# Kernel optimization log

Measured on AMD Instinct MI355X. Metric: run time of the kernel, lower is better.

The kernel has to match this reference:

```python
import jax, jax.numpy as jnp
import numpy as np

N_NODES = 50000
N_EDGES = 400000
N_GRAPHS = 128
IN_DIM = 768
HID = 128
N_CLASSES = 11
BN_EPS = 1e-5


def _sage_conv(x, src, dst, Wl, bl, Wr):
    # PyG SAGEConv (aggr='mean'): out = lin_l(mean_{j->i} x_j) + lin_r(x_i)
    # messages flow src -> dst; nodes with no in-edges get a zero aggregate.
    n = x.shape[0]
    deg = jax.ops.segment_sum(jnp.ones_like(dst, x.dtype), dst, num_segments=n)
    agg = jax.ops.segment_sum(x[src], dst, num_segments=n)  # [N, d] gather+scatter
    agg = agg / jnp.maximum(deg, 1.0)[:, None]
    return agg @ Wl.T + bl + x @ Wr.T


def _batch_norm(x, gamma, beta):
    # training-mode BatchNorm1d: biased batch statistics over the node axis
    m = jnp.mean(x, axis=0)
    v = jnp.var(x, axis=0)
    return (x - m) * jax.lax.rsqrt(v + BN_EPS) * gamma + beta


def setup_inputs() -> dict:
    key = jax.random.key(0)
    ks = jax.random.split(key, 16)
    x = jax.random.normal(ks[0], (N_NODES, IN_DIM), dtype=jnp.float32)
    edge_index = jax.random.randint(ks[1], (2, N_EDGES), 0, N_NODES, dtype=jnp.int32)
    batch = jnp.sort(jax.random.randint(ks[2], (N_NODES,), 0, N_GRAPHS, dtype=jnp.int32))

    def lin_w(k, out_d, in_d):
        return jax.random.normal(k, (out_d, in_d), dtype=jnp.float32) * (1.0 / np.sqrt(in_d))

    params = {
        'W1l': lin_w(ks[3], HID, IN_DIM), 'b1': jnp.zeros((HID,), jnp.float32),
        'W1r': lin_w(ks[4], HID, IN_DIM),
        'g1': jnp.ones((HID,), jnp.float32), 'be1': jnp.zeros((HID,), jnp.float32),
        'W2l': lin_w(ks[5], HID, HID), 'b2': jnp.zeros((HID,), jnp.float32),
        'W2r': lin_w(ks[6], HID, HID),
        'g2': jnp.ones((HID,), jnp.float32), 'be2': jnp.zeros((HID,), jnp.float32),
        'W3l': lin_w(ks[7], HID, HID), 'b3': jnp.zeros((HID,), jnp.float32),
        'W3r': lin_w(ks[8], HID, HID),
        'g3': jnp.ones((HID,), jnp.float32), 'be3': jnp.zeros((HID,), jnp.float32),
        'Wlin': lin_w(ks[9], N_CLASSES, HID), 'blin': jnp.zeros((N_CLASSES,), jnp.float32),
    }
    return {'x': x, 'edge_index': edge_index, 'batch': batch, **params}


def reference(x, edge_index, batch,
              W1l, b1, W1r, g1, be1,
              W2l, b2, W2r, g2, be2,
              W3l, b3, W3r, g3, be3,
              Wlin, blin):
    src, dst = edge_index[0], edge_index[1]
    h = jax.nn.relu(_batch_norm(_sage_conv(x, src, dst, W1l, b1, W1r), g1, be1))
    h = jax.nn.relu(_batch_norm(_sage_conv(h, src, dst, W2l, b2, W2r), g2, be2))
    h = _batch_norm(_sage_conv(h, src, dst, W3l, b3, W3r), g3, be3)
    # global_max_pool over graph ids
    pooled = jax.ops.segment_max(h, batch, num_segments=N_GRAPHS)  # [G, HID]
    # dropout is identity at inference
    return pooled @ Wlin.T + blin  # [G, 11]
```

## Files before the change

kernel.cpp:

```cpp
#include <hip/hip_runtime.h>

#define N_NODESC 50000
#define N_EDGESC 400000
#define N_GRAPHSC 128
#define IN_DIMC 768
#define HIDC 128
#define NCLSC 11
#define BN_EPSC 1e-5f
#define NB_AGG 8
#define NREP 64
#define SCAN_NB ((N_NODESC + 255) / 256)

typedef __bf16 bf16_t;
typedef __bf16 bf16x8 __attribute__((ext_vector_type(8)));
typedef float f32x4 __attribute__((ext_vector_type(4)));

__device__ inline f32x4 mfma_16x16x32_bf16(bf16x8 a, bf16x8 b, f32x4 c) {
    return __builtin_amdgcn_mfma_f32_16x16x32_bf16(a, b, c, 0, 0, 0);
}

template<bool APPLY_BN>
__global__ __launch_bounds__(256) void gemm_kernel(const float* __restrict__ A,
                                                   const float* __restrict__ Bl,
                                                   const float* __restrict__ Br,
                                                   const float* __restrict__ sc,
                                                   bf16_t* __restrict__ Cl,
                                                   float* __restrict__ Cr, int M, int K)
{
    __shared__ bf16_t As[128][40];
    __shared__ bf16_t Bs[128][40];

    const int t  = threadIdx.x;
    const int m0 = blockIdx.x * 128;
    const float* Bsel = (blockIdx.y == 0) ? Bl : Br;

    const int r  = t >> 3;
    const int c4 = (t & 7) * 4;

    const int wid  = t >> 6;
    const int lane = t & 63;
    const int wm   = (wid >> 1) * 64;
    const int wn   = (wid & 1) * 64;
    const int l16  = lane & 15;
    const int quad = lane >> 4;

    f32x4 acc[4][4] = {};

    for (int k0 = 0; k0 < K; k0 += 32) {
#pragma unroll
        for (int p = 0; p < 4; p++) {
            int row = r + p * 32;
            int am  = m0 + row; if (am > M - 1) am = M - 1;
            float4 v = *(const float4*)&A[(size_t)am * K + k0 + c4];
            if (APPLY_BN) {
                float4 s4 = *(const float4*)&sc[k0 + c4];
                float4 h4 = *(const float4*)&sc[HIDC + k0 + c4];
                v.x = fmaxf(fmaf(v.x, s4.x, h4.x), 0.0f);
                v.y = fmaxf(fmaf(v.y, s4.y, h4.y), 0.0f);
                v.z = fmaxf(fmaf(v.z, s4.z, h4.z), 0.0f);
                v.w = fmaxf(fmaf(v.w, s4.w, h4.w), 0.0f);
            }
            As[row][c4 + 0] = (bf16_t)v.x; As[row][c4 + 1] = (bf16_t)v.y;
            As[row][c4 + 2] = (bf16_t)v.z; As[row][c4 + 3] = (bf16_t)v.w;
            float4 w = *(const float4*)&Bsel[(size_t)row * K + k0 + c4];
            Bs[row][c4 + 0] = (bf16_t)w.x; Bs[row][c4 + 1] = (bf16_t)w.y;
            Bs[row][c4 + 2] = (bf16_t)w.z; Bs[row][c4 + 3] = (bf16_t)w.w;
        }
        __syncthreads();

        bf16x8 af[4], bfr[4];
#pragma unroll
        for (int i = 0; i < 4; i++)
            af[i] = *(const bf16x8*)&As[wm + i * 16 + l16][quad * 8];
#pragma unroll
        for (int j = 0; j < 4; j++)
            bfr[j] = *(const bf16x8*)&Bs[wn + j * 16 + l16][quad * 8];
#pragma unroll
        for (int i = 0; i < 4; i++)
#pragma unroll
            for (int j = 0; j < 4; j++)
                acc[i][j] = mfma_16x16x32_bf16(af[i], bfr[j], acc[i][j]);
        __syncthreads();
    }

#pragma unroll
    for (int i = 0; i < 4; i++) {
        int rowb = m0 + wm + i * 16 + quad * 4;
#pragma unroll
        for (int j = 0; j < 4; j++) {
            int colh = wn + j * 16 + l16;
#pragma unroll
            for (int rr = 0; rr < 4; rr++) {
                int row = rowb + rr;
                if (row < M) {
                    if (blockIdx.y == 0) Cl[(size_t)row * HIDC + colh] = (bf16_t)acc[i][j][rr];
                    else                 Cr[(size_t)row * HIDC + colh] = acc[i][j][rr];
                }
            }
        }
    }
}

__global__ void degi_kernel(const int* __restrict__ ei, int* __restrict__ degi) {
    int e = blockIdx.x * blockDim.x + threadIdx.x;
    if (e < N_EDGESC) atomicAdd(&degi[ei[N_EDGESC + e]], 1);
}

__global__ __launch_bounds__(256) void scan1_kernel(const int* __restrict__ degi,
                                                    int* __restrict__ local,
                                                    int* __restrict__ partials)
{
    __shared__ int tmp[256];
    const int t = threadIdx.x;
    const int i = blockIdx.x * 256 + t;
    int v = (i < N_NODESC) ? degi[i] : 0;
    tmp[t] = v;
    __syncthreads();
    for (int off = 1; off < 256; off <<= 1) {
        int u = (t >= off) ? tmp[t - off] : 0;
        __syncthreads();
        tmp[t] += u;
        __syncthreads();
    }
    if (i < N_NODESC) local[i] = tmp[t] - v;
    if (t == 255) partials[blockIdx.x] = tmp[255];
}

__global__ __launch_bounds__(256) void scan2_kernel(int* __restrict__ partials)
{
    __shared__ int tmp[256];
    const int t = threadIdx.x;
    int v = (t < SCAN_NB) ? partials[t] : 0;
    tmp[t] = v;
    __syncthreads();
    for (int off = 1; off < 256; off <<= 1) {
        int u = (t >= off) ? tmp[t - off] : 0;
        __syncthreads();
        tmp[t] += u;
        __syncthreads();
    }
    if (t < SCAN_NB) partials[t] = tmp[t] - v;
}

__global__ __launch_bounds__(256) void scan3_kernel(const int* __restrict__ local,
                                                    const int* __restrict__ partials,
                                                    int* __restrict__ rowptr,
                                                    int* __restrict__ cursor)
{
    const int i = blockIdx.x * 256 + threadIdx.x;
    if (i < N_NODESC) {
        int r = local[i] + partials[blockIdx.x];
        rowptr[i] = r;
        cursor[i] = r;
    }
    if (i == 0) rowptr[N_NODESC] = N_EDGESC;
}

__global__ void fill_kernel(const int* __restrict__ ei, int* __restrict__ cursor,
                            int* __restrict__ col) {
    int e = blockIdx.x * blockDim.x + threadIdx.x;
    if (e >= N_EDGESC) return;
    int d = ei[N_EDGESC + e];
    int pos = atomicAdd(&cursor[d], 1);
    col[pos] = ei[e];
}

__global__ __launch_bounds__(128) void agg_combine_kernel(const int* __restrict__ rowptr,
                                                          const int* __restrict__ col,
                                                          const bf16_t* __restrict__ Plb,
                                                          const float* __restrict__ Pr,
                                                          const float* __restrict__ bias,
                                                          float* __restrict__ Hpre,
                                                          float* __restrict__ stats, int M)
{
    const int c = threadIdx.x;
    const float b = bias[c];
    float s = 0.f, s2 = 0.f;
    const int n0 = blockIdx.x * NB_AGG;
    for (int rr = 0; rr < NB_AGG; rr++) {
        int n = n0 + rr;
        if (n >= M) break;
        int lo = rowptr[n], hi = rowptr[n + 1];
        float a = 0.f;
        for (int e = lo; e < hi; e += 8) {
            int rem = hi - e;
            int idx[8];
#pragma unroll
            for (int j = 0; j < 8; j++) {
                int ee = e + j; if (ee > hi - 1) ee = hi - 1;
                idx[j] = col[ee];
            }
            float v[8];
#pragma unroll
            for (int j = 0; j < 8; j++)
                v[j] = (float)Plb[(size_t)idx[j] * HIDC + c];
#pragma unroll
            for (int j = 0; j < 8; j++)
                if (j < rem) a += v[j];
        }
        int d = hi - lo;
        float inv = 1.0f / (float)(d > 0 ? d : 1);
        float pre = fmaf(a, inv, b) + Pr[(size_t)n * HIDC + c];
        Hpre[(size_t)n * HIDC + c] = pre;
        s += pre; s2 += pre * pre;
    }
    const int rep = blockIdx.x & (NREP - 1);
    atomicAdd(&stats[rep * 256 + c], s);
    atomicAdd(&stats[rep * 256 + HIDC + c], s2);
}

__global__ __launch_bounds__(128) void finalize_kernel(const float* __restrict__ stats,
                                                       const float* __restrict__ g,
                                                       const float* __restrict__ be,
                                                       float* __restrict__ sc, int M)
{
    int c = threadIdx.x;
    float sum = 0.f, sumsq = 0.f;
    for (int r = 0; r < NREP; r++) {
        sum   += stats[r * 256 + c];
        sumsq += stats[r * 256 + HIDC + c];
    }
    float invM = 1.0f / (float)M;
    float mean = sum * invM;
    float var  = sumsq * invM - mean * mean;
    float s = rsqrtf(var + BN_EPSC) * g[c];
    sc[c] = s;
    sc[HIDC + c] = be[c] - mean * s;
}

__global__ __launch_bounds__(128) void pool_kernel(const float* __restrict__ Hpre,
                                                   const float* __restrict__ sc,
                                                   const int* __restrict__ batch,
                                                   float* __restrict__ pooled, int M)
{
    int gph = blockIdx.x;
    int c   = threadIdx.x;
    float s = sc[c], h = sc[HIDC + c];
    int lo = 0, hi = M;
    while (lo < hi) { int m = (lo + hi) >> 1; if (batch[m] < gph) lo = m + 1; else hi = m; }
    int lo2 = lo, hi2 = M;
    while (lo2 < hi2) { int m = (lo2 + hi2) >> 1; if (batch[m] < gph + 1) lo2 = m + 1; else hi2 = m; }
    float mx = -INFINITY;
    for (int rr = lo; rr < lo2; rr++)
        mx = fmaxf(mx, fmaf(Hpre[(size_t)rr * HIDC + c], s, h));
    pooled[gph * HIDC + c] = mx;
}

__global__ __launch_bounds__(128) void final_kernel(const float* __restrict__ pooled,
                                                    const float* __restrict__ W,
                                                    const float* __restrict__ bl,
                                                    float* __restrict__ out)
{
    __shared__ float sp[HIDC];
    int gph = blockIdx.x;
    int t   = threadIdx.x;
    sp[t] = pooled[gph * HIDC + t];
    __syncthreads();
    if (t < NCLSC) {
        float acc = bl[t];
        for (int c = 0; c < HIDC; c++) acc += sp[c] * W[t * HIDC + c];
        out[gph * NCLSC + t] = acc;
    }
}

extern "C" void kernel_launch(void* const* d_in, const int* in_sizes, int n_in,
                              void* d_out, int out_size, void* d_ws, size_t ws_size,
                              hipStream_t stream)
{
    const float* x     = (const float*)d_in[0];
    const int*   ei    = (const int*)d_in[1];
    const int*   batch = (const int*)d_in[2];
    const float* W1l = (const float*)d_in[3];
    const float* b1  = (const float*)d_in[4];
    const float* W1r = (const float*)d_in[5];
    const float* g1  = (const float*)d_in[6];
    const float* be1 = (const float*)d_in[7];
    const float* W2l = (const float*)d_in[8];
    const float* b2  = (const float*)d_in[9];
    const float* W2r = (const float*)d_in[10];
    const float* g2  = (const float*)d_in[11];
    const float* be2 = (const float*)d_in[12];
    const float* W3l = (const float*)d_in[13];
    const float* b3  = (const float*)d_in[14];
    const float* W3r = (const float*)d_in[15];
    const float* g3  = (const float*)d_in[16];
    const float* be3 = (const float*)d_in[17];
    const float* Wlin = (const float*)d_in[18];
    const float* blin = (const float*)d_in[19];

    const int M = N_NODESC;

    char* w = (char*)d_ws;
    bf16_t* Plb  = (bf16_t*)w;  w += (size_t)M * HIDC * 2;
    float* Pr    = (float*)w;   w += (size_t)M * HIDC * 4;
    float* Hpre  = (float*)w;   w += (size_t)M * HIDC * 4;
    int*   rowptr= (int*)w;     w += (size_t)(M + 16) * 4;
    int*   col   = (int*)w;     w += (size_t)N_EDGESC * 4;
    int*   cursor= (int*)w;     w += (size_t)M * 4;
    int*   degi  = (int*)w;     w += (size_t)M * 4;
    int*   slocal= (int*)w;     w += (size_t)M * 4;
    int*   spart = (int*)w;     w += 256 * 4;
    float* stats = (float*)w;   w += (size_t)NREP * 256 * 4;
    float* sc    = (float*)w;   w += 256 * 4;
    float* pooled= (float*)w;   w += (size_t)N_GRAPHSC * HIDC * 4;

    const dim3 gemm_grid((M + 127) / 128, 2);
    const int agg_blocks = (M + NB_AGG - 1) / NB_AGG;
    const size_t stats_bytes = (size_t)NREP * 256 * 4;

    hipMemsetAsync(degi, 0, (size_t)M * 4, stream);
    degi_kernel<<<(N_EDGESC + 255) / 256, 256, 0, stream>>>(ei, degi);
    scan1_kernel<<<SCAN_NB, 256, 0, stream>>>(degi, slocal, spart);
    scan2_kernel<<<1, 256, 0, stream>>>(spart);
    scan3_kernel<<<SCAN_NB, 256, 0, stream>>>(slocal, spart, rowptr, cursor);
    fill_kernel<<<(N_EDGESC + 255) / 256, 256, 0, stream>>>(ei, cursor, col);

    gemm_kernel<false><<<gemm_grid, 256, 0, stream>>>(x, W1l, W1r, nullptr, Plb, Pr, M, IN_DIMC);
    hipMemsetAsync(stats, 0, stats_bytes, stream);
    agg_combine_kernel<<<agg_blocks, 128, 0, stream>>>(rowptr, col, Plb, Pr, b1, Hpre, stats, M);
    finalize_kernel<<<1, 128, 0, stream>>>(stats, g1, be1, sc, M);

    gemm_kernel<true><<<gemm_grid, 256, 0, stream>>>(Hpre, W2l, W2r, sc, Plb, Pr, M, HIDC);
    hipMemsetAsync(stats, 0, stats_bytes, stream);
    agg_combine_kernel<<<agg_blocks, 128, 0, stream>>>(rowptr, col, Plb, Pr, b2, Hpre, stats, M);
    finalize_kernel<<<1, 128, 0, stream>>>(stats, g2, be2, sc, M);

    gemm_kernel<true><<<gemm_grid, 256, 0, stream>>>(Hpre, W3l, W3r, sc, Plb, Pr, M, HIDC);
    hipMemsetAsync(stats, 0, stats_bytes, stream);
    agg_combine_kernel<<<agg_blocks, 128, 0, stream>>>(rowptr, col, Plb, Pr, b3, Hpre, stats, M);
    finalize_kernel<<<1, 128, 0, stream>>>(stats, g3, be3, sc, M);

    pool_kernel<<<N_GRAPHSC, 128, 0, stream>>>(Hpre, sc, batch, pooled, M);
    final_kernel<<<N_GRAPHSC, 128, 0, stream>>>(pooled, Wlin, blin, (float*)d_out);
}
```

Baseline: 595.2 us.

## Load GEMM tiles via global_load_lds with swizzle, store intermediates in bf16

The GEMM now copies A and B tiles straight into swizzled LDS using the global_load_lds builtin. Conversion to bf16 and the BN+ReLU step happen after the LDS read instead of during staging through registers. Weights are converted to bf16 once per call by a small kernel. The right-branch projection and the pre-BN activations are now stored in bf16 instead of fp32, halving the traffic in the aggregation and pooling kernels at some cost in precision.

```diff
diff --git a/kernel.cpp b/kernel.cpp
--- a/kernel.cpp
+++ b/kernel.cpp
@@ -15,28 +15,35 @@
 typedef __bf16 bf16x8 __attribute__((ext_vector_type(8)));
 typedef float f32x4 __attribute__((ext_vector_type(4)));
 
-__device__ inline f32x4 mfma_16x16x32_bf16(bf16x8 a, bf16x8 b, f32x4 c) {
+typedef __attribute__((address_space(1))) void glb_void;
+typedef __attribute__((address_space(3))) void lds_void;
+
+__device__ __forceinline__ void cp16(const void* g, void* l) {
+    __builtin_amdgcn_global_load_lds((glb_void*)g, (lds_void*)l, 16, 0, 0);
+}
+
+__device__ __forceinline__ f32x4 mfma_16x16x32_bf16(bf16x8 a, bf16x8 b, f32x4 c) {
     return __builtin_amdgcn_mfma_f32_16x16x32_bf16(a, b, c, 0, 0, 0);
 }
 
-template<bool APPLY_BN>
-__global__ __launch_bounds__(256) void gemm_kernel(const float* __restrict__ A,
-                                                   const float* __restrict__ Bl,
-                                                   const float* __restrict__ Br,
+template<int MODE>
+__global__ __launch_bounds__(256) void gemm_kernel(const void* __restrict__ Av,
+                                                   const bf16_t* __restrict__ Wb,
                                                    const float* __restrict__ sc,
                                                    bf16_t* __restrict__ Cl,
-                                                   float* __restrict__ Cr, int M, int K)
-{
-    __shared__ bf16_t As[128][40];
-    __shared__ bf16_t Bs[128][40];
-
-    const int t  = threadIdx.x;
-    const int m0 = blockIdx.x * 128;
-    const float* Bsel = (blockIdx.y == 0) ? Bl : Br;
-
-    const int r  = t >> 3;
-    const int c4 = (t & 7) * 4;
-
+                                                   bf16_t* __restrict__ Cr,
+                                                   int M, int K)
+{
+    constexpr int ABYTES = (MODE == 0) ? 128 * 32 * 4 : 128 * 32 * 2;
+    constexpr int AISS   = (MODE == 0) ? 4 : 2;
+    constexpr int AESZ   = (MODE == 0) ? 4 : 2;
+    __shared__ __align__(16) unsigned char smem[ABYTES + 128 * 32 * 2];
+    unsigned char* Asm = smem;
+    unsigned char* Bsm = smem + ABYTES;
+
+    const int t    = threadIdx.x;
+    const int m0   = blockIdx.x * 128;
+    const int half = blockIdx.y;
     const int wid  = t >> 6;
     const int lane = t & 63;
     const int wm   = (wid >> 1) * 64;
@@ -44,37 +51,83 @@
     const int l16  = lane & 15;
     const int quad = lane >> 4;
 
+    const char* aSrc[AISS]; int aDst[AISS];
+#pragma unroll
+    for (int s = 0; s < AISS; s++) {
+        int L = (s * 4 + wid) * 64 + lane;
+        int r, c;
+        if (MODE == 0) { r = L >> 3; c = (L & 7) ^ (r & 7); }
+        else           { r = L >> 2; c = (L & 3) ^ ((r >> 1) & 3); }
+        int row = m0 + r; if (row > M - 1) row = M - 1;
+        aSrc[s] = (const char*)Av + ((size_t)row * K + (size_t)c * (16 / AESZ)) * AESZ;
+        aDst[s] = (s * 4 + wid) * 1024;
+    }
+    const char* bSrc[2]; int bDst[2];
+#pragma unroll
+    for (int s = 0; s < 2; s++) {
+        int L = (s * 4 + wid) * 64 + lane;
+        int r = L >> 2;
+        int c = (L & 3) ^ ((r >> 1) & 3);
+        bSrc[s] = (const char*)(Wb + (size_t)(half * 128 + r) * K + c * 8);
+        bDst[s] = (s * 4 + wid) * 1024;
+    }
+
+    int aOff[4][2], bOff[4];
+#pragma unroll
+    for (int i = 0; i < 4; i++) {
+        int ra = wm + i * 16 + l16;
+        if (MODE == 0) {
+            aOff[i][0] = ra * 128 + (((2 * quad)     ^ (ra & 7)) * 16);
+            aOff[i][1] = ra * 128 + (((2 * quad + 1) ^ (ra & 7)) * 16);
+        } else {
+            aOff[i][0] = ra * 64 + ((quad ^ ((ra >> 1) & 3)) * 16);
+            aOff[i][1] = 0;
+        }
+        int rb = wn + i * 16 + l16;
+        bOff[i] = rb * 64 + ((quad ^ ((rb >> 1) & 3)) * 16);
+    }
+
     f32x4 acc[4][4] = {};
 
     for (int k0 = 0; k0 < K; k0 += 32) {
 #pragma unroll
-        for (int p = 0; p < 4; p++) {
-            int row = r + p * 32;
-            int am  = m0 + row; if (am > M - 1) am = M - 1;
-            float4 v = *(const float4*)&A[(size_t)am * K + k0 + c4];
-            if (APPLY_BN) {
-                float4 s4 = *(const float4*)&sc[k0 + c4];
-                float4 h4 = *(const float4*)&sc[HIDC + k0 + c4];
-                v.x = fmaxf(fmaf(v.x, s4.x, h4.x), 0.0f);
-                v.y = fmaxf(fmaf(v.y, s4.y, h4.y), 0.0f);
-                v.z = fmaxf(fmaf(v.z, s4.z, h4.z), 0.0f);
-                v.w = fmaxf(fmaf(v.w, s4.w, h4.w), 0.0f);
+        for (int s = 0; s < AISS; s++)
+            cp16(aSrc[s] + (size_t)k0 * AESZ, Asm + aDst[s]);
+#pragma unroll
+        for (int s = 0; s < 2; s++)
+            cp16(bSrc[s] + (size_t)k0 * 2, Bsm + bDst[s]);
+        __syncthreads();
+
+        bf16x8 af[4], bfr[4];
+        if (MODE == 0) {
+#pragma unroll
+            for (int i = 0; i < 4; i++) {
+                float4 u0 = *(const float4*)(Asm + aOff[i][0]);
+                float4 u1 = *(const float4*)(Asm + aOff[i][1]);
+                af[i][0] = (bf16_t)u0.x; af[i][1] = (bf16_t)u0.y;
+                af[i][2] = (bf16_t)u0.z; af[i][3] = (bf16_t)u0.w;
+                af[i][4] = (bf16_t)u1.x; af[i][5] = (bf16_t)u1.y;
+                af[i][6] = (bf16_t)u1.z; af[i][7] = (bf16_t)u1.w;
             }
-            As[row][c4 + 0] = (bf16_t)v.x; As[row][c4 + 1] = (bf16_t)v.y;
-            As[row][c4 + 2] = (bf16_t)v.z; As[row][c4 + 3] = (bf16_t)v.w;
-            float4 w = *(const float4*)&Bsel[(size_t)row * K + k0 + c4];
-            Bs[row][c4 + 0] = (bf16_t)w.x; Bs[row][c4 + 1] = (bf16_t)w.y;
-            Bs[row][c4 + 2] = (bf16_t)w.z; Bs[row][c4 + 3] = (bf16_t)w.w;
+        } else {
+            const int ch0 = k0 + quad * 8;
+            float4 s0 = *(const float4*)&sc[ch0];
+            float4 s1 = *(const float4*)&sc[ch0 + 4];
+            float4 h0 = *(const float4*)&sc[HIDC + ch0];
+            float4 h1 = *(const float4*)&sc[HIDC + ch0 + 4];
+            float ss[8] = {s0.x, s0.y, s0.z, s0.w, s1.x, s1.y, s1.z, s1.w};
+            float hh[8] = {h0.x, h0.y, h0.z, h0.w, h1.x, h1.y, h1.z, h1.w};
+#pragma unroll
+            for (int i = 0; i < 4; i++) {
+                bf16x8 raw = *(const bf16x8*)(Asm + aOff[i][0]);
+#pragma unroll
+                for (int e = 0; e < 8; e++)
+                    af[i][e] = (bf16_t)fmaxf(fmaf((float)raw[e], ss[e], hh[e]), 0.0f);
+            }
         }
-        __syncthreads();
-
-        bf16x8 af[4], bfr[4];
-#pragma unroll
-        for (int i = 0; i < 4; i++)
-            af[i] = *(const bf16x8*)&As[wm + i * 16 + l16][quad * 8];
 #pragma unroll
         for (int j = 0; j < 4; j++)
-            bfr[j] = *(const bf16x8*)&Bs[wn + j * 16 + l16][quad * 8];
+            bfr[j] = *(const bf16x8*)(Bsm + bOff[j]);
 #pragma unroll
         for (int i = 0; i < 4; i++)
 #pragma unroll
@@ -83,6 +136,7 @@
         __syncthreads();
     }
 
+    bf16_t* C = half ? Cr : Cl;
 #pragma unroll
     for (int i = 0; i < 4; i++) {
         int rowb = m0 + wm + i * 16 + quad * 4;
@@ -92,13 +146,18 @@
 #pragma unroll
             for (int rr = 0; rr < 4; rr++) {
                 int row = rowb + rr;
-                if (row < M) {
-                    if (blockIdx.y == 0) Cl[(size_t)row * HIDC + colh] = (bf16_t)acc[i][j][rr];
-                    else                 Cr[(size_t)row * HIDC + colh] = acc[i][j][rr];
-                }
+                if (row < M) C[(size_t)row * HIDC + colh] = (bf16_t)acc[i][j][rr];
             }
         }
     }
+}
+
+__global__ void wconv_kernel(const float* __restrict__ Wl, const float* __restrict__ Wr,
+                             bf16_t* __restrict__ out, int KN)
+{
+    int i = blockIdx.x * blockDim.x + threadIdx.x;
+    if (i < KN)           out[i] = (bf16_t)Wl[i];
+    else if (i < 2 * KN)  out[i] = (bf16_t)Wr[i - KN];
 }
 
 __global__ void degi_kernel(const int* __restrict__ ei, int* __restrict__ degi) {
@@ -168,9 +227,9 @@
 __global__ __launch_bounds__(128) void agg_combine_kernel(const int* __restrict__ rowptr,
                                                           const int* __restrict__ col,
                                                           const bf16_t* __restrict__ Plb,
-                                                          const float* __restrict__ Pr,
+                                                          const bf16_t* __restrict__ Prb,
                                                           const float* __restrict__ bias,
-                                                          float* __restrict__ Hpre,
+                                                          bf16_t* __restrict__ Hb,
                                                           float* __restrict__ stats, int M)
 {
     const int c = threadIdx.x;
@@ -200,8 +259,8 @@
         }
         int d = hi - lo;
         float inv = 1.0f / (float)(d > 0 ? d : 1);
-        float pre = fmaf(a, inv, b) + Pr[(size_t)n * HIDC + c];
-        Hpre[(size_t)n * HIDC + c] = pre;
+        float pre = fmaf(a, inv, b) + (float)Prb[(size_t)n * HIDC + c];
+        Hb[(size_t)n * HIDC + c] = (bf16_t)pre;
         s += pre; s2 += pre * pre;
     }
     const int rep = blockIdx.x & (NREP - 1);
@@ -228,7 +287,7 @@
     sc[HIDC + c] = be[c] - mean * s;
 }
 
-__global__ __launch_bounds__(128) void pool_kernel(const float* __restrict__ Hpre,
+__global__ __launch_bounds__(128) void pool_kernel(const bf16_t* __restrict__ Hb,
                                                    const float* __restrict__ sc,
                                                    const int* __restrict__ batch,
                                                    float* __restrict__ pooled, int M)
@@ -242,7 +301,7 @@
     while (lo2 < hi2) { int m = (lo2 + hi2) >> 1; if (batch[m] < gph + 1) lo2 = m + 1; else hi2 = m; }
     float mx = -INFINITY;
     for (int rr = lo; rr < lo2; rr++)
-        mx = fmaxf(mx, fmaf(Hpre[(size_t)rr * HIDC + c], s, h));
+        mx = fmaxf(mx, fmaf((float)Hb[(size_t)rr * HIDC + c], s, h));
     pooled[gph * HIDC + c] = mx;
 }
 
@@ -292,8 +351,11 @@
 
     char* w = (char*)d_ws;
     bf16_t* Plb  = (bf16_t*)w;  w += (size_t)M * HIDC * 2;
-    float* Pr    = (float*)w;   w += (size_t)M * HIDC * 4;
-    float* Hpre  = (float*)w;   w += (size_t)M * HIDC * 4;
+    bf16_t* Prb  = (bf16_t*)w;  w += (size_t)M * HIDC * 2;
+    bf16_t* Hb   = (bf16_t*)w;  w += (size_t)M * HIDC * 2;
+    bf16_t* Wb1  = (bf16_t*)w;  w += (size_t)256 * IN_DIMC * 2;
+    bf16_t* Wb2  = (bf16_t*)w;  w += (size_t)256 * HIDC * 2;
+    bf16_t* Wb3  = (bf16_t*)w;  w += (size_t)256 * HIDC * 2;
     int*   rowptr= (int*)w;     w += (size_t)(M + 16) * 4;
     int*   col   = (int*)w;     w += (size_t)N_EDGESC * 4;
     int*   cursor= (int*)w;     w += (size_t)M * 4;
@@ -308,6 +370,10 @@
     const int agg_blocks = (M + NB_AGG - 1) / NB_AGG;
     const size_t stats_bytes = (size_t)NREP * 256 * 4;
 
+    wconv_kernel<<<(2 * 128 * IN_DIMC + 255) / 256, 256, 0, stream>>>(W1l, W1r, Wb1, 128 * IN_DIMC);
+    wconv_kernel<<<(2 * 128 * HIDC + 255) / 256, 256, 0, stream>>>(W2l, W2r, Wb2, 128 * HIDC);
+    wconv_kernel<<<(2 * 128 * HIDC + 255) / 256, 256, 0, stream>>>(W3l, W3r, Wb3, 128 * HIDC);
+
     hipMemsetAsync(degi, 0, (size_t)M * 4, stream);
     degi_kernel<<<(N_EDGESC + 255) / 256, 256, 0, stream>>>(ei, degi);
     scan1_kernel<<<SCAN_NB, 256, 0, stream>>>(degi, slocal, spart);
@@ -315,21 +381,21 @@
     scan3_kernel<<<SCAN_NB, 256, 0, stream>>>(slocal, spart, rowptr, cursor);
     fill_kernel<<<(N_EDGESC + 255) / 256, 256, 0, stream>>>(ei, cursor, col);
 
-    gemm_kernel<false><<<gemm_grid, 256, 0, stream>>>(x, W1l, W1r, nullptr, Plb, Pr, M, IN_DIMC);
+    gemm_kernel<0><<<gemm_grid, 256, 0, stream>>>(x, Wb1, nullptr, Plb, Prb, M, IN_DIMC);
     hipMemsetAsync(stats, 0, stats_bytes, stream);
-    agg_combine_kernel<<<agg_blocks, 128, 0, stream>>>(rowptr, col, Plb, Pr, b1, Hpre, stats, M);
+    agg_combine_kernel<<<agg_blocks, 128, 0, stream>>>(rowptr, col, Plb, Prb, b1, Hb, stats, M);
     finalize_kernel<<<1, 128, 0, stream>>>(stats, g1, be1, sc, M);
 
-    gemm_kernel<true><<<gemm_grid, 256, 0, stream>>>(Hpre, W2l, W2r, sc, Plb, Pr, M, HIDC);
+    gemm_kernel<1><<<gemm_grid, 256, 0, stream>>>(Hb, Wb2, sc, Plb, Prb, M, HIDC);
     hipMemsetAsync(stats, 0, stats_bytes, stream);
-    agg_combine_kernel<<<agg_blocks, 128, 0, stream>>>(rowptr, col, Plb, Pr, b2, Hpre, stats, M);
+    agg_combine_kernel<<<agg_blocks, 128, 0, stream>>>(rowptr, col, Plb, Prb, b2, Hb, stats, M);
     finalize_kernel<<<1, 128, 0, stream>>>(stats, g2, be2, sc, M);
 
-    gemm_kernel<true><<<gemm_grid, 256, 0, stream>>>(Hpre, W3l, W3r, sc, Plb, Pr, M, HIDC);
+    gemm_kernel<1><<<gemm_grid, 256, 0, stream>>>(Hb, Wb3, sc, Plb, Prb, M, HIDC);
     hipMemsetAsync(stats, 0, stats_bytes, stream);
-    agg_combine_kernel<<<agg_blocks, 128, 0, stream>>>(rowptr, col, Plb, Pr, b3, Hpre, stats, M);
+    agg_combine_kernel<<<agg_blocks, 128, 0, stream>>>(rowptr, col, Plb, Prb, b3, Hb, stats, M);
     finalize_kernel<<<1, 128, 0, stream>>>(stats, g3, be3, sc, M);
 
-    pool_kernel<<<N_GRAPHSC, 128, 0, stream>>>(Hpre, sc, batch, pooled, M);
+    pool_kernel<<<N_GRAPHSC, 128, 0, stream>>>(Hb, sc, batch, pooled, M);
     final_kernel<<<N_GRAPHSC, 128, 0, stream>>>(pooled, Wlin, blin, (float*)d_out);
 }
```

Measured after the change: 584.3 us. No clear change (-1.8%).
